# Kernel optimization log

Hardware: AMD Instinct MI355X
Metric: run time of the kernel (lower is better)

## Reference

```python
import jax, jax.numpy as jnp
import numpy as np

N = 50000
E = 600000


def setup_inputs() -> dict:
    key = jax.random.key(0)
    ks = jax.random.split(key, 8)
    x = jax.random.normal(ks[0], (N, 128), dtype=jnp.float32)
    # guarantee every node appears at least once as a source (row) so deg > 0
    row_extra = jax.random.randint(ks[1], (E - N,), 0, N, dtype=jnp.int32)
    row = jnp.concatenate([jnp.arange(N, dtype=jnp.int32), row_extra])
    col = jax.random.randint(ks[2], (E,), 0, N, dtype=jnp.int32)
    edge_index = jnp.stack([row, col])  # [2, E]
    edge_weight = jax.random.uniform(ks[3], (E,), dtype=jnp.float32, minval=0.1, maxval=1.0)
    s1 = 1.0 / np.sqrt(128)
    W1 = jax.random.normal(ks[4], (128, 128), dtype=jnp.float32) * s1
    b1 = jnp.zeros((128,), dtype=jnp.float32)
    W2 = jax.random.normal(ks[5], (128, 128), dtype=jnp.float32) * s1
    b2 = jnp.zeros((128,), dtype=jnp.float32)
    return {"x": x, "edge_index": edge_index, "edge_weight": edge_weight,
            "W1": W1, "b1": b1, "W2": W2, "b2": b2}


def _gcn_layer(x, row, col, edge_weight, W, b):
    # dense linear (torch Linear: x @ W.T + b)
    h = x @ W.T + b  # [N, d_out]
    n = h.shape[0]
    # degree via scatter-add of edge weights over source nodes
    deg = jax.ops.segment_sum(edge_weight, row, num_segments=n)  # [N]
    deg_inv_sqrt = deg ** -0.5
    norm = deg_inv_sqrt[row] * edge_weight * deg_inv_sqrt[col]  # [E]
    # message: gather source features, scale, scatter-add to targets
    msg = norm[:, None] * h[row]  # [E, d_out]
    return jax.ops.segment_sum(msg, col, num_segments=n)  # [N, d_out]


def reference(x, edge_index, edge_weight, W1, b1, W2, b2):
    row, col = edge_index[0], edge_index[1]
    h = _gcn_layer(x, row, col, edge_weight, W1, b1)
    h = jax.nn.relu(h)
    return _gcn_layer(h, row, col, edge_weight, W2, b2)
```

## Files before the change

### kernel.cpp

```cpp
#include <hip/hip_runtime.h>

#define DF 128
#define CAP 40
#define TROWS 64

__device__ __forceinline__ float4 agg_node(const float4* __restrict__ H4,
                                           const int2* __restrict__ bucket,
                                           int m, const float* __restrict__ deg,
                                           int t)
{
    float4 acc = make_float4(0.f, 0.f, 0.f, 0.f);
    int i = 0;
    for (; i + 4 <= m; i += 4) {
        const int4* b4 = (const int4*)(bucket + i);
        const int4 p0 = b4[0];
        const int4 p1 = b4[1];
        const float w0 = __int_as_float(p0.y) * rsqrtf(deg[p0.x]);
        const float w1 = __int_as_float(p0.w) * rsqrtf(deg[p0.z]);
        const float w2 = __int_as_float(p1.y) * rsqrtf(deg[p1.x]);
        const float w3 = __int_as_float(p1.w) * rsqrtf(deg[p1.z]);
        const float4 h0 = H4[(size_t)p0.x * 32 + t];
        const float4 h1 = H4[(size_t)p0.z * 32 + t];
        const float4 h2 = H4[(size_t)p1.x * 32 + t];
        const float4 h3 = H4[(size_t)p1.z * 32 + t];
        acc.x = fmaf(w0, h0.x, acc.x);
        acc.y = fmaf(w0, h0.y, acc.y);
        acc.z = fmaf(w0, h0.z, acc.z);
        acc.w = fmaf(w0, h0.w, acc.w);
        acc.x = fmaf(w1, h1.x, acc.x);
        acc.y = fmaf(w1, h1.y, acc.y);
        acc.z = fmaf(w1, h1.z, acc.z);
        acc.w = fmaf(w1, h1.w, acc.w);
        acc.x = fmaf(w2, h2.x, acc.x);
        acc.y = fmaf(w2, h2.y, acc.y);
        acc.z = fmaf(w2, h2.z, acc.z);
        acc.w = fmaf(w2, h2.w, acc.w);
        acc.x = fmaf(w3, h3.x, acc.x);
        acc.y = fmaf(w3, h3.y, acc.y);
        acc.z = fmaf(w3, h3.z, acc.z);
        acc.w = fmaf(w3, h3.w, acc.w);
    }
    for (; i < m; ++i) {
        const int2 rec = bucket[i];
        const float wv = __int_as_float(rec.y) * rsqrtf(deg[rec.x]);
        const float4 h = H4[(size_t)rec.x * 32 + t];
        acc.x = fmaf(wv, h.x, acc.x);
        acc.y = fmaf(wv, h.y, acc.y);
        acc.z = fmaf(wv, h.z, acc.z);
        acc.w = fmaf(wv, h.w, acc.w);
    }
    return acc;
}

__device__ __forceinline__ void gemm_from_lds(
    float* __restrict__ Xs, float* __restrict__ Wsk,
    const float* __restrict__ W, const float* __restrict__ b,
    float* __restrict__ H, int nrows, int n0, int tid)
{
    const int rgrp = tid >> 5;
    const int cgrp = tid & 31;

    float4 acc[8];
    const float4 bias = ((const float4*)b)[cgrp];
#pragma unroll
    for (int r = 0; r < 8; ++r) acc[r] = bias;

    const float4* Xs4 = (const float4*)Xs;
    const float4* Ws4 = (const float4*)Wsk;

    for (int k0 = 0; k0 < DF; k0 += 32) {
        __syncthreads();
#pragma unroll
        for (int i = 0; i < 4; ++i) {
            int idx = tid + i * 256;
            int c   = idx >> 3;
            int kk  = idx & 7;
            float4 v = ((const float4*)(W + (size_t)c * DF + k0))[kk];
            int kb = kk * 4;
            Wsk[(kb + 0) * DF + c] = v.x;
            Wsk[(kb + 1) * DF + c] = v.y;
            Wsk[(kb + 2) * DF + c] = v.z;
            Wsk[(kb + 3) * DF + c] = v.w;
        }
        __syncthreads();

#pragma unroll
        for (int kk = 0; kk < 8; ++kk) {
            const int kb = (k0 >> 2) + kk;
            float4 w0 = Ws4[(kk * 4 + 0) * 32 + cgrp];
            float4 w1 = Ws4[(kk * 4 + 1) * 32 + cgrp];
            float4 w2 = Ws4[(kk * 4 + 2) * 32 + cgrp];
            float4 w3 = Ws4[(kk * 4 + 3) * 32 + cgrp];
#pragma unroll
            for (int r = 0; r < 8; ++r) {
                float4 x4 = Xs4[(rgrp * 8 + r) * 32 + kb];
                acc[r].x = fmaf(x4.x, w0.x, acc[r].x);
                acc[r].y = fmaf(x4.x, w0.y, acc[r].y);
                acc[r].z = fmaf(x4.x, w0.z, acc[r].z);
                acc[r].w = fmaf(x4.x, w0.w, acc[r].w);
                acc[r].x = fmaf(x4.y, w1.x, acc[r].x);
                acc[r].y = fmaf(x4.y, w1.y, acc[r].y);
                acc[r].z = fmaf(x4.y, w1.z, acc[r].z);
                acc[r].w = fmaf(x4.y, w1.w, acc[r].w);
                acc[r].x = fmaf(x4.z, w2.x, acc[r].x);
                acc[r].y = fmaf(x4.z, w2.y, acc[r].y);
                acc[r].z = fmaf(x4.z, w2.z, acc[r].z);
                acc[r].w = fmaf(x4.z, w2.w, acc[r].w);
                acc[r].x = fmaf(x4.w, w3.x, acc[r].x);
                acc[r].y = fmaf(x4.w, w3.y, acc[r].y);
                acc[r].z = fmaf(x4.w, w3.z, acc[r].z);
                acc[r].w = fmaf(x4.w, w3.w, acc[r].w);
            }
        }
    }

#pragma unroll
    for (int r = 0; r < 8; ++r) {
        int n = n0 + rgrp * 8 + r;
        if (n < nrows) ((float4*)(H + (size_t)n * DF))[cgrp] = acc[r];
    }
}

__global__ __launch_bounds__(256) void build_gemm_kernel(
    const float* __restrict__ X, const float* __restrict__ W,
    const float* __restrict__ b, float* __restrict__ H, int nrows,
    const int* __restrict__ row, const int* __restrict__ col,
    const float* __restrict__ ew,
    float* __restrict__ deg, int* __restrict__ cnt, int2* __restrict__ csr,
    int E, int gemmBlocks)
{
    __shared__ float Xs[TROWS * DF];
    __shared__ float Wsk[32 * DF];

    const int tid = threadIdx.x;

    if (blockIdx.x >= gemmBlocks) {
        int e = (blockIdx.x - gemmBlocks) * 256 + tid;
        if (e < E) {
            int r = row[e], c = col[e];
            float wv = ew[e];
            atomicAdd(&deg[r], wv);
            int pos = atomicAdd(&cnt[c], 1);
            if (pos < CAP)
                csr[(size_t)c * CAP + pos] = make_int2(r, __float_as_int(wv));
        }
        return;
    }

    const int n0 = blockIdx.x * TROWS;
#pragma unroll
    for (int i = 0; i < 8; ++i) {
        int idx = tid + i * 256;
        int r   = idx >> 5;
        int kk  = idx & 31;
        int n   = n0 + r;
        float4 v = make_float4(0.f, 0.f, 0.f, 0.f);
        if (n < nrows) v = ((const float4*)(X + (size_t)n * DF))[kk];
        ((float4*)Xs)[idx] = v;
    }
    gemm_from_lds(Xs, Wsk, W, b, H, nrows, n0, tid);
}

__global__ __launch_bounds__(256) void agg_gemm_kernel(
    const float4* __restrict__ H4,
    const int2* __restrict__ csr, const int* __restrict__ cnt,
    const float* __restrict__ deg,
    const float* __restrict__ W, const float* __restrict__ b,
    float* __restrict__ O, int N)
{
    __shared__ float Xs[TROWS * DF];
    __shared__ float Wsk[32 * DF];

    const int tid = threadIdx.x;
    const int g   = tid >> 5;
    const int t   = tid & 31;
    const int n0  = blockIdx.x * TROWS;

#pragma unroll
    for (int j = 0; j < 8; ++j) {
        const int r    = g * 8 + j;
        const int node = n0 + r;
        float4 acc = make_float4(0.f, 0.f, 0.f, 0.f);
        if (node < N) {
            int m = cnt[node];
            if (m > CAP) m = CAP;
            const int2* bucket = csr + (size_t)node * CAP;
            acc = agg_node(H4, bucket, m, deg, t);
            const float dcol = rsqrtf(deg[node]);
            acc.x = fmaxf(acc.x * dcol, 0.f);
            acc.y = fmaxf(acc.y * dcol, 0.f);
            acc.z = fmaxf(acc.z * dcol, 0.f);
            acc.w = fmaxf(acc.w * dcol, 0.f);
        }
        ((float4*)Xs)[r * 32 + t] = acc;
    }
    gemm_from_lds(Xs, Wsk, W, b, O, N, n0, tid);
}

__global__ void agg_kernel(const float4* __restrict__ H4,
                           const int2* __restrict__ csr, const int* __restrict__ cnt,
                           const float* __restrict__ deg,
                           float4* __restrict__ O4, int N)
{
    const int gid  = blockIdx.x * blockDim.x + threadIdx.x;
    const int node = gid >> 5;
    const int t    = gid & 31;
    if (node >= N) return;
    int m = cnt[node];
    if (m > CAP) m = CAP;
    const int2* bucket = csr + (size_t)node * CAP;
    float4 acc = agg_node(H4, bucket, m, deg, t);
    const float dcol = rsqrtf(deg[node]);
    acc.x *= dcol; acc.y *= dcol; acc.z *= dcol; acc.w *= dcol;
    O4[(size_t)node * 32 + t] = acc;
}

extern "C" void kernel_launch(void* const* d_in, const int* in_sizes, int n_in,
                              void* d_out, int out_size, void* d_ws, size_t ws_size,
                              hipStream_t stream) {
    const float* x  = (const float*)d_in[0];
    const int*   ei = (const int*)d_in[1];
    const float* ew = (const float*)d_in[2];
    const float* W1 = (const float*)d_in[3];
    const float* b1 = (const float*)d_in[4];
    const float* W2 = (const float*)d_in[5];
    const float* b2 = (const float*)d_in[6];
    float* out = (float*)d_out;

    const int E = in_sizes[2];
    const int N = in_sizes[0] / DF;
    const int* row = ei;
    const int* col = ei + E;

    char* ws = (char*)d_ws;
    size_t offb = 0;
    auto alloc = [&](size_t bytes) { char* p = ws + offb; offb = (offb + bytes + 511) & ~(size_t)511; return p; };
    float* deg  = (float*)alloc((size_t)2 * N * 4);
    int*   cnt  = (int*)(deg + N);
    int2*  csr  = (int2*)alloc((size_t)N * CAP * 8);
    float* h1   = (float*)alloc((size_t)N * DF * 4);
    float* h2   = (float*)alloc((size_t)N * DF * 4);
    (void)ws_size;

    hipMemsetAsync(deg, 0, (size_t)2 * N * 4, stream);

    const int TB = 256;
    const int eblocks = (E + TB - 1) / TB;
    const int gemm_blocks = (N + TROWS - 1) / TROWS;

    build_gemm_kernel<<<gemm_blocks + eblocks, 256, 0, stream>>>(
        x, W1, b1, h1, N, row, col, ew, deg, cnt, csr, E, gemm_blocks);

    agg_gemm_kernel<<<gemm_blocks, 256, 0, stream>>>(
        (const float4*)h1, csr, cnt, deg, W2, b2, h2, N);

    const int agg_blocks = (N * 32 + TB - 1) / TB;
    agg_kernel<<<agg_blocks, TB, 0, stream>>>((const float4*)h2, csr, cnt, deg,
                                              (float4*)out, N);
}
```

Before: 305.3 us.

## Interleave two nodes per warp in aggregation and halve agg-GEMM tile rows

The aggregation loops now process two destination nodes together, issuing eight independent row gathers per iteration to raise memory-level parallelism. The fused aggregate+GEMM kernel uses 32-row tiles with 4 rows per thread and a launch-bounds occupancy hint of 4 blocks, which halves LDS use and doubles the block count. The final aggregation kernel uses half as many threads, each handling a node pair. The trade-offs are more register pressure and reloading W2 into LDS for twice as many blocks.

```diff
diff --git a/kernel.cpp b/kernel.cpp
--- a/kernel.cpp
+++ b/kernel.cpp
@@ -2,56 +2,86 @@
 
 #define DF 128
 #define CAP 40
-#define TROWS 64
-
-__device__ __forceinline__ float4 agg_node(const float4* __restrict__ H4,
+
+#define FMA4(a4, s, v)                                              \
+    a4.x = fmaf(s, v.x, a4.x); a4.y = fmaf(s, v.y, a4.y);           \
+    a4.z = fmaf(s, v.z, a4.z); a4.w = fmaf(s, v.w, a4.w)
+
+__device__ __forceinline__ float4 agg_tail(const float4* __restrict__ H4,
                                            const int2* __restrict__ bucket,
-                                           int m, const float* __restrict__ deg,
-                                           int t)
-{
-    float4 acc = make_float4(0.f, 0.f, 0.f, 0.f);
-    int i = 0;
+                                           int i, int m,
+                                           const float* __restrict__ deg,
+                                           int t, float4 acc)
+{
     for (; i + 4 <= m; i += 4) {
         const int4* b4 = (const int4*)(bucket + i);
         const int4 p0 = b4[0];
         const int4 p1 = b4[1];
-        const float w0 = __int_as_float(p0.y) * rsqrtf(deg[p0.x]);
-        const float w1 = __int_as_float(p0.w) * rsqrtf(deg[p0.z]);
-        const float w2 = __int_as_float(p1.y) * rsqrtf(deg[p1.x]);
-        const float w3 = __int_as_float(p1.w) * rsqrtf(deg[p1.z]);
         const float4 h0 = H4[(size_t)p0.x * 32 + t];
         const float4 h1 = H4[(size_t)p0.z * 32 + t];
         const float4 h2 = H4[(size_t)p1.x * 32 + t];
         const float4 h3 = H4[(size_t)p1.z * 32 + t];
-        acc.x = fmaf(w0, h0.x, acc.x);
-        acc.y = fmaf(w0, h0.y, acc.y);
-        acc.z = fmaf(w0, h0.z, acc.z);
-        acc.w = fmaf(w0, h0.w, acc.w);
-        acc.x = fmaf(w1, h1.x, acc.x);
-        acc.y = fmaf(w1, h1.y, acc.y);
-        acc.z = fmaf(w1, h1.z, acc.z);
-        acc.w = fmaf(w1, h1.w, acc.w);
-        acc.x = fmaf(w2, h2.x, acc.x);
-        acc.y = fmaf(w2, h2.y, acc.y);
-        acc.z = fmaf(w2, h2.z, acc.z);
-        acc.w = fmaf(w2, h2.w, acc.w);
-        acc.x = fmaf(w3, h3.x, acc.x);
-        acc.y = fmaf(w3, h3.y, acc.y);
-        acc.z = fmaf(w3, h3.z, acc.z);
-        acc.w = fmaf(w3, h3.w, acc.w);
+        const float s0 = __int_as_float(p0.y) * rsqrtf(deg[p0.x]);
+        const float s1 = __int_as_float(p0.w) * rsqrtf(deg[p0.z]);
+        const float s2 = __int_as_float(p1.y) * rsqrtf(deg[p1.x]);
+        const float s3 = __int_as_float(p1.w) * rsqrtf(deg[p1.z]);
+        FMA4(acc, s0, h0);
+        FMA4(acc, s1, h1);
+        FMA4(acc, s2, h2);
+        FMA4(acc, s3, h3);
     }
     for (; i < m; ++i) {
         const int2 rec = bucket[i];
-        const float wv = __int_as_float(rec.y) * rsqrtf(deg[rec.x]);
-        const float4 h = H4[(size_t)rec.x * 32 + t];
-        acc.x = fmaf(wv, h.x, acc.x);
-        acc.y = fmaf(wv, h.y, acc.y);
-        acc.z = fmaf(wv, h.z, acc.z);
-        acc.w = fmaf(wv, h.w, acc.w);
+        const float sv = __int_as_float(rec.y) * rsqrtf(deg[rec.x]);
+        const float4 hv = H4[(size_t)rec.x * 32 + t];
+        FMA4(acc, sv, hv);
     }
     return acc;
 }
 
+__device__ __forceinline__ void agg2(const float4* __restrict__ H4,
+                                     const int2* __restrict__ bA, int mA,
+                                     const int2* __restrict__ bB, int mB,
+                                     const float* __restrict__ deg, int t,
+                                     float4& accA, float4& accB)
+{
+    const int mc = mA < mB ? mA : mB;
+    int i = 0;
+    for (; i + 4 <= mc; i += 4) {
+        const int4 a0 = ((const int4*)(bA + i))[0];
+        const int4 a1 = ((const int4*)(bA + i))[1];
+        const int4 c0 = ((const int4*)(bB + i))[0];
+        const int4 c1 = ((const int4*)(bB + i))[1];
+        const float4 hA0 = H4[(size_t)a0.x * 32 + t];
+        const float4 hA1 = H4[(size_t)a0.z * 32 + t];
+        const float4 hA2 = H4[(size_t)a1.x * 32 + t];
+        const float4 hA3 = H4[(size_t)a1.z * 32 + t];
+        const float4 hB0 = H4[(size_t)c0.x * 32 + t];
+        const float4 hB1 = H4[(size_t)c0.z * 32 + t];
+        const float4 hB2 = H4[(size_t)c1.x * 32 + t];
+        const float4 hB3 = H4[(size_t)c1.z * 32 + t];
+        const float sA0 = __int_as_float(a0.y) * rsqrtf(deg[a0.x]);
+        const float sA1 = __int_as_float(a0.w) * rsqrtf(deg[a0.z]);
+        const float sA2 = __int_as_float(a1.y) * rsqrtf(deg[a1.x]);
+        const float sA3 = __int_as_float(a1.w) * rsqrtf(deg[a1.z]);
+        const float sB0 = __int_as_float(c0.y) * rsqrtf(deg[c0.x]);
+        const float sB1 = __int_as_float(c0.w) * rsqrtf(deg[c0.z]);
+        const float sB2 = __int_as_float(c1.y) * rsqrtf(deg[c1.x]);
+        const float sB3 = __int_as_float(c1.w) * rsqrtf(deg[c1.z]);
+        FMA4(accA, sA0, hA0);
+        FMA4(accA, sA1, hA1);
+        FMA4(accA, sA2, hA2);
+        FMA4(accA, sA3, hA3);
+        FMA4(accB, sB0, hB0);
+        FMA4(accB, sB1, hB1);
+        FMA4(accB, sB2, hB2);
+        FMA4(accB, sB3, hB3);
+    }
+    accA = agg_tail(H4, bA, i, mA, deg, t, accA);
+    accB = agg_tail(H4, bB, i, mB, deg, t, accB);
+}
+
+template <int RPT>
 __device__ __forceinline__ void gemm_from_lds(
     float* __restrict__ Xs, float* __restrict__ Wsk,
     const float* __restrict__ W, const float* __restrict__ b,
@@ -60,10 +90,10 @@
     const int rgrp = tid >> 5;
     const int cgrp = tid & 31;
 
-    float4 acc[8];
+    float4 acc[RPT];
     const float4 bias = ((const float4*)b)[cgrp];
 #pragma unroll
-    for (int r = 0; r < 8; ++r) acc[r] = bias;
+    for (int r = 0; r < RPT; ++r) acc[r] = bias;
 
     const float4* Xs4 = (const float4*)Xs;
     const float4* Ws4 = (const float4*)Wsk;
@@ -92,8 +122,8 @@
             float4 w2 = Ws4[(kk * 4 + 2) * 32 + cgrp];
             float4 w3 = Ws4[(kk * 4 + 3) * 32 + cgrp];
 #pragma unroll
-            for (int r = 0; r < 8; ++r) {
-                float4 x4 = Xs4[(rgrp * 8 + r) * 32 + kb];
+            for (int r = 0; r < RPT; ++r) {
+                float4 x4 = Xs4[(rgrp * RPT + r) * 32 + kb];
                 acc[r].x = fmaf(x4.x, w0.x, acc[r].x);
                 acc[r].y = fmaf(x4.x, w0.y, acc[r].y);
                 acc[r].z = fmaf(x4.x, w0.z, acc[r].z);
@@ -115,8 +145,8 @@
     }
 
 #pragma unroll
-    for (int r = 0; r < 8; ++r) {
-        int n = n0 + rgrp * 8 + r;
+    for (int r = 0; r < RPT; ++r) {
+        int n = n0 + rgrp * RPT + r;
         if (n < nrows) ((float4*)(H + (size_t)n * DF))[cgrp] = acc[r];
     }
 }
@@ -129,7 +159,7 @@
     float* __restrict__ deg, int* __restrict__ cnt, int2* __restrict__ csr,
     int E, int gemmBlocks)
 {
-    __shared__ float Xs[TROWS * DF];
+    __shared__ float Xs[64 * DF];
     __shared__ float Wsk[32 * DF];
 
     const int tid = threadIdx.x;
@@ -147,7 +177,7 @@
         return;
     }
 
-    const int n0 = blockIdx.x * TROWS;
+    const int n0 = blockIdx.x * 64;
 #pragma unroll
     for (int i = 0; i < 8; ++i) {
         int idx = tid + i * 256;
@@ -158,61 +188,80 @@
         if (n < nrows) v = ((const float4*)(X + (size_t)n * DF))[kk];
         ((float4*)Xs)[idx] = v;
     }
-    gemm_from_lds(Xs, Wsk, W, b, H, nrows, n0, tid);
-}
-
-__global__ __launch_bounds__(256) void agg_gemm_kernel(
+    gemm_from_lds<8>(Xs, Wsk, W, b, H, nrows, n0, tid);
+}
+
+__global__ __launch_bounds__(256, 4) void agg_gemm_kernel(
     const float4* __restrict__ H4,
     const int2* __restrict__ csr, const int* __restrict__ cnt,
     const float* __restrict__ deg,
     const float* __restrict__ W, const float* __restrict__ b,
     float* __restrict__ O, int N)
 {
-    __shared__ float Xs[TROWS * DF];
+    __shared__ float Xs[32 * DF];
     __shared__ float Wsk[32 * DF];
 
     const int tid = threadIdx.x;
     const int g   = tid >> 5;
     const int t   = tid & 31;
-    const int n0  = blockIdx.x * TROWS;
-
-#pragma unroll
-    for (int j = 0; j < 8; ++j) {
-        const int r    = g * 8 + j;
-        const int node = n0 + r;
-        float4 acc = make_float4(0.f, 0.f, 0.f, 0.f);
-        if (node < N) {
-            int m = cnt[node];
-            if (m > CAP) m = CAP;
-            const int2* bucket = csr + (size_t)node * CAP;
-            acc = agg_node(H4, bucket, m, deg, t);
-            const float dcol = rsqrtf(deg[node]);
-            acc.x = fmaxf(acc.x * dcol, 0.f);
-            acc.y = fmaxf(acc.y * dcol, 0.f);
-            acc.z = fmaxf(acc.z * dcol, 0.f);
-            acc.w = fmaxf(acc.w * dcol, 0.f);
-        }
-        ((float4*)Xs)[r * 32 + t] = acc;
-    }
-    gemm_from_lds(Xs, Wsk, W, b, O, N, n0, tid);
-}
-
-__global__ void agg_kernel(const float4* __restrict__ H4,
-                           const int2* __restrict__ csr, const int* __restrict__ cnt,
-                           const float* __restrict__ deg,
-                           float4* __restrict__ O4, int N)
+    const int n0  = blockIdx.x * 32;
+
+#pragma unroll
+    for (int jp = 0; jp < 2; ++jp) {
+        const int rA = g * 4 + jp * 2;
+        const int rB = rA + 1;
+        const int nodeA = n0 + rA;
+        const int nodeB = n0 + rB;
+        int mA = 0, mB = 0;
+        if (nodeA < N) { mA = cnt[nodeA]; if (mA > CAP) mA = CAP; }
+        if (nodeB < N) { mB = cnt[nodeB]; if (mB > CAP) mB = CAP; }
+        float4 accA = make_float4(0.f, 0.f, 0.f, 0.f);
+        float4 accB = make_float4(0.f, 0.f, 0.f, 0.f);
+        agg2(H4, csr + (size_t)nodeA * CAP, mA,
+                 csr + (size_t)nodeB * CAP, mB, deg, t, accA, accB);
+        if (nodeA < N) {
+            const float d = rsqrtf(deg[nodeA]);
+            accA.x = fmaxf(accA.x * d, 0.f); accA.y = fmaxf(accA.y * d, 0.f);
+            accA.z = fmaxf(accA.z * d, 0.f); accA.w = fmaxf(accA.w * d, 0.f);
+        }
+        if (nodeB < N) {
+            const float d = rsqrtf(deg[nodeB]);
+            accB.x = fmaxf(accB.x * d, 0.f); accB.y = fmaxf(accB.y * d, 0.f);
+            accB.z = fmaxf(accB.z * d, 0.f); accB.w = fmaxf(accB.w * d, 0.f);
+        }
+        ((float4*)Xs)[rA * 32 + t] = accA;
+        ((float4*)Xs)[rB * 32 + t] = accB;
+    }
+    gemm_from_lds<4>(Xs, Wsk, W, b, O, N, n0, tid);
+}
+
+__global__ __launch_bounds__(256) void agg_kernel(
+    const float4* __restrict__ H4,
+    const int2* __restrict__ csr, const int* __restrict__ cnt,
+    const float* __restrict__ deg,
+    float4* __restrict__ O4, int N)
 {
     const int gid  = blockIdx.x * blockDim.x + threadIdx.x;
-    const int node = gid >> 5;
+    const int half = gid >> 5;
     const int t    = gid & 31;
-    if (node >= N) return;
-    int m = cnt[node];
-    if (m > CAP) m = CAP;
-    const int2* bucket = csr + (size_t)node * CAP;
-    float4 acc = agg_node(H4, bucket, m, deg, t);
-    const float dcol = rsqrtf(deg[node]);
-    acc.x *= dcol; acc.y *= dcol; acc.z *= dcol; acc.w *= dcol;
-    O4[(size_t)node * 32 + t] = acc;
+    const int nA   = half * 2;
+    const int nB   = nA + 1;
+    if (nA >= N) return;
+    int mA = cnt[nA]; if (mA > CAP) mA = CAP;
+    int mB = 0;
+    if (nB < N) { mB = cnt[nB]; if (mB > CAP) mB = CAP; }
+    float4 accA = make_float4(0.f, 0.f, 0.f, 0.f);
+    float4 accB = make_float4(0.f, 0.f, 0.f, 0.f);
+    agg2(H4, csr + (size_t)nA * CAP, mA,
+             csr + (size_t)nB * CAP, mB, deg, t, accA, accB);
+    const float dA = rsqrtf(deg[nA]);
+    accA.x *= dA; accA.y *= dA; accA.z *= dA; accA.w *= dA;
+    O4[(size_t)nA * 32 + t] = accA;
+    if (nB < N) {
+        const float dB = rsqrtf(deg[nB]);
+        accB.x *= dB; accB.y *= dB; accB.z *= dB; accB.w *= dB;
+        O4[(size_t)nB * 32 + t] = accB;
+    }
 }
 
 extern "C" void kernel_launch(void* const* d_in, const int* in_sizes, int n_in,
@@ -246,15 +295,17 @@
 
     const int TB = 256;
     const int eblocks = (E + TB - 1) / TB;
-    const int gemm_blocks = (N + TROWS - 1) / TROWS;
-
-    build_gemm_kernel<<<gemm_blocks + eblocks, 256, 0, stream>>>(
-        x, W1, b1, h1, N, row, col, ew, deg, cnt, csr, E, gemm_blocks);
-
-    agg_gemm_kernel<<<gemm_blocks, 256, 0, stream>>>(
+    const int gemm1_blocks = (N + 63) / 64;
+    const int agg_gemm_blocks = (N + 31) / 32;
+
+    build_gemm_kernel<<<gemm1_blocks + eblocks, 256, 0, stream>>>(
+        x, W1, b1, h1, N, row, col, ew, deg, cnt, csr, E, gemm1_blocks);
+
+    agg_gemm_kernel<<<agg_gemm_blocks, 256, 0, stream>>>(
         (const float4*)h1, csr, cnt, deg, W2, b2, h2, N);
 
-    const int agg_blocks = (N * 32 + TB - 1) / TB;
+    const int pairs = (N + 1) / 2;
+    const int agg_blocks = (pairs * 32 + TB - 1) / TB;
     agg_kernel<<<agg_blocks, TB, 0, stream>>>((const float4*)h2, csr, cnt, deg,
                                               (float4*)out, N);
 }
```

After: 281.6 us. 7.8% less time.
